# Performance work log

Measured on AMD Instinct MI355X. Metric: run time of the kernel, lower is better.

The kernel has to match this reference:

```python
import jax, jax.numpy as jnp
import numpy as np

N, K, H, HEADS, DE, MULT = 8000, 32, 256, 8, 128, 2
DH = H // HEADS
BIG_NEG = -1e9


def _ln(x, g, b):
    mu = x.mean(-1, keepdims=True)
    var = ((x - mu) ** 2).mean(-1, keepdims=True)
    return (x - mu) * jax.lax.rsqrt(var + 1e-5) * g + b


def setup_inputs() -> dict:
    key = jax.random.key(0)
    ks = iter(jax.random.split(key, 64))
    def w(shape, s=0.05):
        return (jax.random.normal(next(ks), shape, jnp.float32) * s)
    stdv = float(np.sqrt(6.0 / (HEADS + DH)))
    inp = {
        'node_features': jax.random.normal(next(ks), (N, H), jnp.float32),
        'edge_features': jax.random.normal(next(ks), (N, K, H), jnp.float32),
        'edge_attr_raw': jax.random.normal(next(ks), (N, K, DE), jnp.float32),
        'angle_embedding': jax.random.normal(next(ks), (N, HEADS, K, K), jnp.float32) * 0.1,
        'ln1n_g': jnp.ones((H,)), 'ln1n_b': jnp.zeros((H,)),
        'ln1e_g': jnp.ones((H,)), 'ln1e_b': jnp.zeros((H,)),
        'W_ea': w((DE, H)), 'b_ea': jnp.zeros((H,)),
        'W_nh': w((H, H)), 'b_nh': jnp.zeros((H,)),
        'W_eh': w((H, H)), 'b_eh': jnp.zeros((H,)),
        'W_gate': w((2 * H, H)), 'b_gate': jnp.zeros((H,)),
        'W_cand': w((2 * H, H)), 'b_cand': jnp.zeros((H,)),
        'attn_scalar': jnp.ones((HEADS,)),
        'W_in': w((H, 3 * H)), 'b_in': jnp.zeros((3 * H,)),
        'W_out': w((H, H)), 'b_out': jnp.zeros((H,)),
        'attn_weight': jax.random.uniform(next(ks), (HEADS, DH), jnp.float32, -stdv, stdv),
        'ln2n_g': jnp.ones((H,)), 'ln2n_b': jnp.zeros((H,)),
        'ln2e_g': jnp.ones((H,)), 'ln2e_b': jnp.zeros((H,)),
        'Wn1': w((H, MULT * H)), 'bn1': jnp.zeros((MULT * H,)),
        'Wn2': w((MULT * H, H)), 'bn2': jnp.zeros((H,)),
        'We1': w((H, MULT * H)), 'be1': jnp.zeros((MULT * H,)),
        'We2': w((MULT * H, H)), 'be2': jnp.zeros((H,)),
        'neighbor_list': jax.random.randint(next(ks), (N, K), 0, N),
        'neighbor_counts': jax.random.randint(next(ks), (N,), 1, K + 1),
    }
    return inp


def _forward(node_features, edge_features, edge_attr_raw, angle_embedding,
             ln1n_g, ln1n_b, ln1e_g, ln1e_b,
             W_ea, b_ea, W_nh, b_nh, W_eh, b_eh,
             W_gate, b_gate, W_cand, b_cand,
             attn_scalar, W_in, b_in, W_out, b_out, attn_weight,
             ln2n_g, ln2n_b, ln2e_g, ln2e_b,
             Wn1, bn1, Wn2, bn2, We1, be1, We2, be2,
             neighbor_list, neighbor_counts):
    mask = jnp.arange(K)[None, :] < neighbor_counts[:, None]  # [N,K] valid neighbors
    # norm_attn
    nh = _ln(node_features, ln1n_g, ln1n_b)
    eh = _ln(edge_features, ln1e_g, ln1e_b)
    # message construction
    edge_attr = jax.nn.gelu(edge_attr_raw @ W_ea + b_ea)            # [N,K,H]
    nbr = nh[neighbor_list]                                          # gather [N,K,H]
    node_hidden = jax.nn.gelu(nbr @ W_nh + b_nh)
    edge_hidden = jax.nn.gelu(eh @ W_eh + b_eh)
    m = jnp.concatenate([edge_attr, node_hidden], axis=-1)          # [N,K,2H]
    gate = jax.nn.sigmoid(m @ W_gate + b_gate)
    cand = jnp.tanh(m @ W_cand + b_cand)
    message = gate * cand + (1.0 - gate) * edge_hidden              # [N,K,H]
    # additive mask: key padding + per-head scaled angle embedding
    attn_mask = jnp.where(mask[:, None, None, :], 0.0, BIG_NEG) \
        + angle_embedding * attn_scalar[None, :, None, None]        # [N,heads,K,K]
    # multi-head self attention over the neighbor dimension
    qkv = message @ W_in + b_in                                     # [N,K,3H]
    q, k, v = jnp.split(qkv, 3, axis=-1)
    q = q.reshape(N, K, HEADS, DH)
    k = k.reshape(N, K, HEADS, DH)
    v = v.reshape(N, K, HEADS, DH)
    scores = jnp.einsum('nqhd,nkhd->nhqk', q, k) / np.float32(np.sqrt(DH)) + attn_mask
    probs = jax.nn.softmax(scores, axis=-1)
    ctx = jnp.einsum('nhqk,nkhd->nqhd', probs, v).reshape(N, K, H)
    edge_output = ctx @ W_out + b_out                               # [N,K,H]
    # graph-attention aggregation to nodes
    eo = edge_output.reshape(N, K, HEADS, DH)
    alpha = (eo * attn_weight[None, None]).sum(-1)                  # [N,K,heads]
    alpha = jax.nn.leaky_relu(alpha, 0.2)
    alpha = jnp.where(mask[:, :, None], alpha, BIG_NEG)
    alpha = jax.nn.softmax(alpha, axis=1)
    node_output = (alpha[..., None] * eo).sum(1).reshape(N, H)
    # residual + FFN
    node_f = node_output + node_features
    edge_f = edge_output + edge_features
    nh2 = _ln(node_f, ln2n_g, ln2n_b)
    eh2 = _ln(edge_f, ln2e_g, ln2e_b)
    node_f = node_f + (jax.nn.gelu(nh2 @ Wn1 + bn1) @ Wn2 + bn2)
    edge_f = edge_f + (jax.nn.gelu(eh2 @ We1 + be1) @ We2 + be2)
    return node_f, edge_f


def reference(node_features, edge_features, edge_attr_raw, angle_embedding,
              ln1n_g, ln1n_b, ln1e_g, ln1e_b,
              W_ea, b_ea, W_nh, b_nh, W_eh, b_eh,
              W_gate, b_gate, W_cand, b_cand,
              attn_scalar, W_in, b_in, W_out, b_out, attn_weight,
              ln2n_g, ln2n_b, ln2e_g, ln2e_b,
              Wn1, bn1, Wn2, bn2, We1, be1, We2, be2,
              neighbor_list, neighbor_counts):
    return _forward(node_features, edge_features, edge_attr_raw, angle_embedding,
                    ln1n_g, ln1n_b, ln1e_g, ln1e_b,
                    W_ea, b_ea, W_nh, b_nh, W_eh, b_eh,
                    W_gate, b_gate, W_cand, b_cand,
                    attn_scalar, W_in, b_in, W_out, b_out, attn_weight,
                    ln2n_g, ln2n_b, ln2e_g, ln2e_b,
                    Wn1, bn1, Wn2, bn2, We1, be1, We2, be2,
                    neighbor_list, neighbor_counts)
```

## Files before the change

### kernel.cpp

```cpp
#include <hip/hip_runtime.h>
#include <math.h>

#define NN 8000
#define KK 32
#define HH 256
#define DE 128
#define NODES 4
#define THREADS 512
#define BIGLD 536
#define LDS_BYTES (128 * BIGLD * 2)

typedef __attribute__((ext_vector_type(8))) short bs8;
typedef __attribute__((ext_vector_type(4))) short bs4;
typedef __attribute__((ext_vector_type(4))) float f4;

#define LGK_FENCE() do { asm volatile("s_waitcnt lgkmcnt(0)" ::: "memory"); __builtin_amdgcn_sched_barrier(0); } while (0)

struct P {
  const float *nf, *ef, *ear, *ang;
  const float *ln1e_g, *ln1e_b;
  const float *b_ea, *b_nh, *b_eh, *b_gate, *b_cand;
  const float *ascal, *b_in, *b_out, *aw;
  const float *ln2n_g, *ln2n_b, *ln2e_g, *ln2e_b;
  const float *bn1, *bn2, *be1, *be2;
  const int *nbrl, *nbrc;
  const unsigned short *nhb;
  const unsigned short *wtEA, *wtNH, *wtEH, *wtG, *wtC, *wtIN, *wtOUT, *wtN1, *wtN2, *wtE1, *wtE2;
  float *on, *oe;
};

__device__ __forceinline__ unsigned short f2b(float f) {
  unsigned int u = __float_as_uint(f);
  unsigned int r = (u + 0x7fffu + ((u >> 16) & 1u)) >> 16;
  return (unsigned short)r;
}
__device__ __forceinline__ float b2f(unsigned short u) {
  return __uint_as_float(((unsigned int)u) << 16);
}
__device__ __forceinline__ unsigned int cvt_pk_bf16(float lo, float hi) {
  unsigned int r;
  asm("v_cvt_pk_bf16_f32 %0, %1, %2" : "=v"(r) : "v"(lo), "v"(hi));
  return r;
}
__device__ __forceinline__ bs4 pack4(float a, float b, float c, float d) {
  union { unsigned int u[2]; bs4 v; } x;
  x.u[0] = cvt_pk_bf16(a, b);
  x.u[1] = cvt_pk_bf16(c, d);
  return x.v;
}
__device__ __forceinline__ float fast_tanh(float x) {
  x = fminf(fmaxf(x, -12.f), 12.f);
  float e = __expf(2.f * x);
  return (e - 1.f) / (e + 1.f);
}
__device__ __forceinline__ float gelu_f(float x) {
  return 0.5f * x * (1.f + fast_tanh(0.7978845608f * (x + 0.044715f * x * x * x)));
}
__device__ __forceinline__ float sigmoid_f(float x) {
  return 1.f / (1.f + __expf(-x));
}

template<int RT, int NCT, int KB, int KW>
__device__ __forceinline__ void gemmB(f4 acc[RT][NCT],
    const unsigned short* __restrict__ wt,
    const unsigned short* __restrict__ A, int cs, int l)
{
  const int lm = l & 15;
  const int lg = (l >> 4) << 3;
  #pragma unroll
  for (int kb = 0; kb < KB; ++kb) {
    bs8 wfr[NCT];
    #pragma unroll
    for (int ct = 0; ct < NCT; ++ct)
      wfr[ct] = *(const bs8*)(wt + (size_t)(cs + ct * 16 + lm) * KW + kb * 32 + lg);
    bs8 afr[RT];
    #pragma unroll
    for (int rt = 0; rt < RT; ++rt)
      afr[rt] = *(const bs8*)(A + (rt * 16 + lm) * BIGLD + kb * 32 + lg);
    #pragma unroll
    for (int rt = 0; rt < RT; ++rt)
      #pragma unroll
      for (int ct = 0; ct < NCT; ++ct)
        acc[rt][ct] = __builtin_amdgcn_mfma_f32_16x16x32_bf16(wfr[ct], afr[rt], acc[rt][ct], 0, 0, 0);
  }
}

template<int RT, int NCT>
__device__ __forceinline__ void zero_acc(f4 acc[RT][NCT]) {
  #pragma unroll
  for (int rt = 0; rt < RT; ++rt)
    #pragma unroll
    for (int ct = 0; ct < NCT; ++ct) {
      acc[rt][ct][0] = 0.f; acc[rt][ct][1] = 0.f; acc[rt][ct][2] = 0.f; acc[rt][ct][3] = 0.f;
    }
}

template<int RT, int NCT, int ACTF>
__device__ __forceinline__ void storeB(unsigned short* dst,
    f4 acc[RT][NCT], const float* __restrict__ bias, int cs, int l)
{
  const int lm = l & 15;
  const int lr = (l >> 4) << 2;
  #pragma unroll
  for (int ct = 0; ct < NCT; ++ct) {
    f4 bv = *(const f4*)(bias + cs + ct * 16 + lr);
    #pragma unroll
    for (int rt = 0; rt < RT; ++rt) {
      float v[4];
      #pragma unroll
      for (int r = 0; r < 4; ++r) {
        v[r] = acc[rt][ct][r] + bv[r];
        if (ACTF == 1) v[r] = gelu_f(v[r]);
      }
      *(bs4*)(dst + (rt * 16 + lm) * BIGLD + cs + ct * 16 + lr) = pack4(v[0], v[1], v[2], v[3]);
    }
  }
}

__global__ void node_ln_bf16(const float* __restrict__ x, const float* __restrict__ g,
                             const float* __restrict__ b, unsigned short* __restrict__ y)
{
  int row = blockIdx.x * 4 + (threadIdx.x >> 6);
  int lane = threadIdx.x & 63;
  float4 v = ((const float4*)(x + (size_t)row * HH))[lane];
  float s = v.x + v.y + v.z + v.w;
  float ss = v.x * v.x + v.y * v.y + v.z * v.z + v.w * v.w;
  #pragma unroll
  for (int m = 1; m < 64; m <<= 1) { s += __shfl_xor(s, m); ss += __shfl_xor(ss, m); }
  float mean = s * (1.f / HH);
  float var = ss * (1.f / HH) - mean * mean;
  float rstd = rsqrtf(var + 1e-5f);
  float4 gg = ((const float4*)g)[lane];
  float4 bb = ((const float4*)b)[lane];
  *(bs4*)(y + (size_t)row * HH + lane * 4) =
      pack4((v.x - mean) * rstd * gg.x + bb.x, (v.y - mean) * rstd * gg.y + bb.y,
            (v.z - mean) * rstd * gg.z + bb.z, (v.w - mean) * rstd * gg.w + bb.w);
}

__global__ void wt_transpose(const float* __restrict__ src, unsigned short* __restrict__ dst,
                             int K, int C)
{
  __shared__ float tile[32][33];
  int tx = threadIdx.x & 31, ty = threadIdx.x >> 5;
  int bk = blockIdx.x, bc = blockIdx.y;
  #pragma unroll
  for (int i = 0; i < 4; ++i)
    tile[ty + i * 8][tx] = src[(size_t)(bk * 32 + ty + i * 8) * C + bc * 32 + tx];
  __syncthreads();
  #pragma unroll
  for (int i = 0; i < 4; ++i)
    dst[(size_t)(bc * 32 + ty + i * 8) * K + bk * 32 + tx] = f2b(tile[tx][ty + i * 8]);
}

__launch_bounds__(THREADS, 2)
__global__ void mega_kernel(P p)
{
  extern __shared__ unsigned short smem[];

  const int tid = threadIdx.x;
  const int l = tid & 63;
  const int w = tid >> 6;
  const int lm = l & 15;
  const int lg = (l >> 4) << 3;
  const int lr = (l >> 4) << 2;
  const int n0 = blockIdx.x * NODES;
  const size_t ebase = (size_t)blockIdx.x * 128;
  const int4 cnt4 = *(const int4*)(p.nbrc + n0);
  const int cnts[4] = { cnt4.x, cnt4.y, cnt4.z, cnt4.w };

  #define FSA(i)  (*(float*)(smem + ((i) >> 7) * BIGLD + 256 + (((i) & 127) << 1)))
  #define FSNF(i) (*(float*)(smem + (8 + ((i) >> 7)) * BIGLD + 256 + (((i) & 127) << 1)))
  #define FLNP(j) (*(float*)(smem + 16 * BIGLD + 256 + ((j) << 1)))

  {
    int row = tid >> 2, q = tid & 3;
    const float* src = p.ear + (ebase + row) * DE + q * 32;
    unsigned short* d = smem + row * BIGLD + q * 32;
    #pragma unroll
    for (int j = 0; j < 8; ++j) {
      float4 v = ((const float4*)src)[j];
      *(bs4*)(d + j * 4) = pack4(v.x, v.y, v.z, v.w);
    }
  }
  __syncthreads();
  {
    f4 acc[8][2]; zero_acc<8,2>(acc);
    gemmB<8,2,4,128>(acc, p.wtEA, smem, w * 32, l);
    __syncthreads();
    storeB<8,2,1>(smem, acc, p.b_ea, w * 32, l);
  }
  __syncthreads();
  {
    int row = tid >> 2, q = tid & 3;
    int idx = p.nbrl[(n0 + (row >> 5)) * KK + (row & 31)];
    const unsigned short* src = p.nhb + (size_t)idx * HH + q * 64;
    unsigned short* d = smem + row * BIGLD + 264 + q * 64;
    #pragma unroll
    for (int j = 0; j < 8; ++j) *(bs8*)(d + j * 8) = *(const bs8*)(src + j * 8);
  }
  __syncthreads();
  {
    f4 acc[8][2]; zero_acc<8,2>(acc);
    gemmB<8,2,8,256>(acc, p.wtNH, smem + 264, w * 32, l);
    __syncthreads();
    storeB<8,2,1>(smem + 256, acc, p.b_nh, w * 32, l);
  }
  __syncthreads();
  bs4 gp[8][2], cp[8][2];
  {
    f4 ga[8][2]; zero_acc<8,2>(ga);
    f4 ca[8][2]; zero_acc<8,2>(ca);
    gemmB<8,2,16,512>(ga, p.wtG, smem, w * 32, l);
    gemmB<8,2,16,512>(ca, p.wtC, smem, w * 32, l);
    #pragma unroll
    for (int ct = 0; ct < 2; ++ct) {
      f4 bg = *(const f4*)(p.b_gate + w * 32 + ct * 16 + lr);
      f4 bc = *(const f4*)(p.b_cand + w * 32 + ct * 16 + lr);
      #pragma unroll
      for (int rt = 0; rt < 8; ++rt) {
        gp[rt][ct] = pack4(sigmoid_f(ga[rt][ct][0] + bg[0]), sigmoid_f(ga[rt][ct][1] + bg[1]),
                           sigmoid_f(ga[rt][ct][2] + bg[2]), sigmoid_f(ga[rt][ct][3] + bg[3]));
        cp[rt][ct] = pack4(fast_tanh(ca[rt][ct][0] + bc[0]), fast_tanh(ca[rt][ct][1] + bc[1]),
                           fast_tanh(ca[rt][ct][2] + bc[2]), fast_tanh(ca[rt][ct][3] + bc[3]));
      }
    }
  }
  __syncthreads();
  {
    int row = tid >> 2, q = tid & 3;
    const float* src = p.ef + (ebase + row) * HH + q * 64;
    float s = 0.f, ss = 0.f;
    #pragma unroll
    for (int j = 0; j < 16; ++j) {
      float4 v = ((const float4*)src)[j];
      s += v.x + v.y + v.z + v.w;
      ss += v.x * v.x + v.y * v.y + v.z * v.z + v.w * v.w;
    }
    s += __shfl_xor(s, 1); ss += __shfl_xor(ss, 1);
    s += __shfl_xor(s, 2); ss += __shfl_xor(ss, 2);
    float mean = s * (1.f / HH);
    float var = ss * (1.f / HH) - mean * mean;
    float rstd = rsqrtf(var + 1e-5f);
    unsigned short* d = smem + row * BIGLD + q * 64;
    #pragma unroll
    for (int j = 0; j < 16; ++j) {
      float4 v = ((const float4*)src)[j];
      int c = q * 64 + j * 4;
      float4 g = *(const float4*)(p.ln1e_g + c);
      float4 b = *(const float4*)(p.ln1e_b + c);
      *(bs4*)(d + j * 4) = pack4((v.x - mean) * rstd * g.x + b.x,
                                 (v.y - mean) * rstd * g.y + b.y,
                                 (v.z - mean) * rstd * g.z + b.z,
                                 (v.w - mean) * rstd * g.w + b.w);
    }
  }
  __syncthreads();
  {
    f4 ea[8][2]; zero_acc<8,2>(ea);
    gemmB<8,2,8,256>(ea, p.wtEH, smem, w * 32, l);
    __syncthreads();
    #pragma unroll
    for (int ct = 0; ct < 2; ++ct) {
      f4 be = *(const f4*)(p.b_eh + w * 32 + ct * 16 + lr);
      #pragma unroll
      for (int rt = 0; rt < 8; ++rt) {
        float o[4];
        #pragma unroll
        for (int r = 0; r < 4; ++r) {
          float g = b2f((unsigned short)gp[rt][ct][r]);
          float c = b2f((unsigned short)cp[rt][ct][r]);
          float eh = gelu_f(ea[rt][ct][r] + be[r]);
          o[r] = g * c + (1.f - g) * eh;
        }
        *(bs4*)(smem + (rt * 16 + lm) * BIGLD + w * 32 + ct * 16 + lr) = pack4(o[0], o[1], o[2], o[3]);
      }
    }
  }
  __syncthreads();
  bs4 qp[8][2], kp[8][2], vp[8][2];
  {
    f4 acc[8][2];
    zero_acc<8,2>(acc);
    gemmB<8,2,8,256>(acc, p.wtIN, smem, w * 32, l);
    #pragma unroll
    for (int ct = 0; ct < 2; ++ct) {
      f4 bv = *(const f4*)(p.b_in + w * 32 + ct * 16 + lr);
      #pragma unroll
      for (int rt = 0; rt < 8; ++rt)
        qp[rt][ct] = pack4(acc[rt][ct][0] + bv[0], acc[rt][ct][1] + bv[1],
                           acc[rt][ct][2] + bv[2], acc[rt][ct][3] + bv[3]);
    }
    zero_acc<8,2>(acc);
    gemmB<8,2,8,256>(acc, p.wtIN + 256 * 256, smem, w * 32, l);
    #pragma unroll
    for (int ct = 0; ct < 2; ++ct) {
      f4 bv = *(const f4*)(p.b_in + 256 + w * 32 + ct * 16 + lr);
      #pragma unroll
      for (int rt = 0; rt < 8; ++rt)
        kp[rt][ct] = pack4(acc[rt][ct][0] + bv[0], acc[rt][ct][1] + bv[1],
                           acc[rt][ct][2] + bv[2], acc[rt][ct][3] + bv[3]);
    }
    zero_acc<8,2>(acc);
    gemmB<8,2,8,256>(acc, p.wtIN + 512 * 256, smem, w * 32, l);
    #pragma unroll
    for (int ct = 0; ct < 2; ++ct) {
      f4 bv = *(const f4*)(p.b_in + 512 + w * 32 + ct * 16 + lr);
      #pragma unroll
      for (int rt = 0; rt < 8; ++rt)
        vp[rt][ct] = pack4(acc[rt][ct][0] + bv[0], acc[rt][ct][1] + bv[1],
                           acc[rt][ct][2] + bv[2], acc[rt][ct][3] + bv[3]);
    }
  }
  __syncthreads();
  bs4 cxp[NODES][2][2];
  {
    const float asc = p.ascal[w];
    f4 z; z[0] = 0.f; z[1] = 0.f; z[2] = 0.f; z[3] = 0.f;
    #define WSADDR(a, r, c) ((w * 8 + (a) * 4 + ((r) >> 3)) * BIGLD + 256 + (((r) & 7) << 5) + (c))
    #pragma unroll
    for (int ni = 0; ni < NODES; ++ni) {
      #pragma unroll
      for (int j = 0; j < 2; ++j)
        #pragma unroll
        for (int ct = 0; ct < 2; ++ct) {
          *(bs4*)(smem + WSADDR(0, j * 16 + lm, ct * 16 + lr)) = qp[2 * ni + j][ct];
          *(bs4*)(smem + WSADDR(1, j * 16 + lm, ct * 16 + lr)) = kp[2 * ni + j][ct];
        }
      LGK_FENCE();
      bs8 qf[2], kf[2];
      #pragma unroll
      for (int t = 0; t < 2; ++t) {
        qf[t] = *(const bs8*)(smem + WSADDR(0, t * 16 + lm, lg));
        kf[t] = *(const bs8*)(smem + WSADDR(1, t * 16 + lm, lg));
      }
      f4 sc[2][2];
      #pragma unroll
      for (int kt = 0; kt < 2; ++kt)
        #pragma unroll
        for (int qt = 0; qt < 2; ++qt)
          sc[kt][qt] = __builtin_amdgcn_mfma_f32_16x16x32_bf16(kf[kt], qf[qt], z, 0, 0, 0);
      float inv[2];
      #pragma unroll
      for (int qt = 0; qt < 2; ++qt) {
        const int q = qt * 16 + lm;
        float sv[2][4];
        #pragma unroll
        for (int kt = 0; kt < 2; ++kt) {
          f4 av = *(const f4*)(p.ang + ((((size_t)(n0 + ni)) * 8 + w) * 32 + q) * 32 + kt * 16 + lr);
          #pragma unroll
          for (int r = 0; r < 4; ++r) {
            int kidx = kt * 16 + lr + r;
            sv[kt][r] = sc[kt][qt][r] * 0.17677669529663687f + av[r] * asc
                      + (kidx < cnts[ni] ? 0.f : -1e9f);
          }
        }
        float m = sv[0][0];
        #pragma unroll
        for (int r = 1; r < 4; ++r) m = fmaxf(m, sv[0][r]);
        #pragma unroll
        for (int r = 0; r < 4; ++r) m = fmaxf(m, sv[1][r]);
        m = fmaxf(m, __shfl_xor(m, 16));
        m = fmaxf(m, __shfl_xor(m, 32));
        float e[2][4], sum = 0.f;
        #pragma unroll
        for (int kt = 0; kt < 2; ++kt)
          #pragma unroll
          for (int r = 0; r < 4; ++r) { e[kt][r] = __expf(sv[kt][r] - m); sum += e[kt][r]; }
        sum += __shfl_xor(sum, 16);
        sum += __shfl_xor(sum, 32);
        inv[qt] = 1.f / sum;
        *(bs4*)(smem + WSADDR(0, q, lr))      = pack4(e[0][0], e[0][1], e[0][2], e[0][3]);
        *(bs4*)(smem + WSADDR(0, q, 16 + lr)) = pack4(e[1][0], e[1][1], e[1][2], e[1][3]);
      }
      #pragma unroll
      for (int j = 0; j < 2; ++j)
        #pragma unroll
        for (int ct = 0; ct < 2; ++ct)
          #pragma unroll
          for (int r = 0; r < 4; ++r)
            smem[WSADDR(1, ct * 16 + lr + r, j * 16 + lm)] = (unsigned short)vp[2 * ni + j][ct][r];
      LGK_FENCE();
      bs8 pf[2], vf[2];
      #pragma unroll
      for (int t = 0; t < 2; ++t) {
        pf[t] = *(const bs8*)(smem + WSADDR(0, t * 16 + lm, lg));
        vf[t] = *(const bs8*)(smem + WSADDR(1, t * 16 + lm, lg));
      }
      #pragma unroll
      for (int qt = 0; qt < 2; ++qt)
        #pragma unroll
        for (int dt = 0; dt < 2; ++dt) {
          f4 cx = __builtin_amdgcn_mfma_f32_16x16x32_bf16(vf[dt], pf[qt], z, 0, 0, 0);
          cxp[ni][qt][dt] = pack4(cx[0] * inv[qt], cx[1] * inv[qt], cx[2] * inv[qt], cx[3] * inv[qt]);
        }
    }
    #undef WSADDR
  }
  __syncthreads();
  {
    #pragma unroll
    for (int ni = 0; ni < NODES; ++ni)
      #pragma unroll
      for (int qt = 0; qt < 2; ++qt)
        #pragma unroll
        for (int dt = 0; dt < 2; ++dt)
          *(bs4*)(smem + (ni * 32 + qt * 16 + lm) * BIGLD + 256 + w * 32 + dt * 16 + lr) = cxp[ni][qt][dt];
  }
  __syncthreads();
  {
    f4 acc[8][2]; zero_acc<8,2>(acc);
    gemmB<8,2,8,256>(acc, p.wtOUT, smem + 256, w * 32, l);
    __syncthreads();
    storeB<8,2,0>(smem, acc, p.b_out, w * 32, l);
  }
  __syncthreads();
  {
    #pragma unroll
    for (int it = 0; it < 2; ++it) {
      int idx = tid + it * 512;
      int ni = idx >> 8, rem = idx & 255;
      int k = rem >> 3, h = rem & 7;
      float aa = 0.f;
      #pragma unroll
      for (int j = 0; j < 8; ++j) {
        bs4 ev = *(const bs4*)(smem + (ni * 32 + k) * BIGLD + h * 32 + j * 4);
        float4 av = *(const float4*)(p.aw + h * 32 + j * 4);
        aa += b2f((unsigned short)ev[0]) * av.x + b2f((unsigned short)ev[1]) * av.y
            + b2f((unsigned short)ev[2]) * av.z + b2f((unsigned short)ev[3]) * av.w;
      }
      aa = aa > 0.f ? aa : 0.2f * aa;
      if (k >= cnts[ni]) aa = -1e9f;
      FSA(idx) = aa;
    }
  }
  __syncthreads();
  {
    int ni = tid >> 7, h = (tid >> 4) & 7, l16 = tid & 15;
    float v0 = FSA(ni * 256 + l16 * 8 + h);
    float v1 = FSA(ni * 256 + (l16 + 16) * 8 + h);
    float m = fmaxf(v0, v1);
    m = fmaxf(m, __shfl_xor(m, 1));
    m = fmaxf(m, __shfl_xor(m, 2));
    m = fmaxf(m, __shfl_xor(m, 4));
    m = fmaxf(m, __shfl_xor(m, 8));
    float e0 = __expf(v0 - m), e1 = __expf(v1 - m);
    float s = e0 + e1;
    s += __shfl_xor(s, 1);
    s += __shfl_xor(s, 2);
    s += __shfl_xor(s, 4);
    s += __shfl_xor(s, 8);
    float inv = 1.f / s;
    FSA(ni * 256 + l16 * 8 + h) = e0 * inv;
    FSA(ni * 256 + (l16 + 16) * 8 + h) = e1 * inv;
  }
  __syncthreads();
  float ndf[2];
  {
    #pragma unroll
    for (int it = 0; it < 2; ++it) {
      int idx = it * 512 + tid;
      int ni = idx >> 8, c = idx & 255, h = c >> 5;
      float no = 0.f;
      #pragma unroll
      for (int k = 0; k < 32; ++k)
        no = fmaf(FSA(ni * 256 + k * 8 + h), b2f(smem[(ni * 32 + k) * BIGLD + c]), no);
      float nodef = no + p.nf[(size_t)(n0 + ni) * HH + c];
      ndf[it] = nodef;
      FSNF(idx) = nodef;
      float s = nodef, ss = nodef * nodef;
      #pragma unroll
      for (int m = 1; m < 64; m <<= 1) { s += __shfl_xor(s, m); ss += __shfl_xor(ss, m); }
      if (l == 0) { FLNP(it * 8 + w) = s; FLNP(16 + it * 8 + w) = ss; }
    }
  }
  __syncthreads();
  {
    #pragma unroll
    for (int it = 0; it < 2; ++it) {
      int idx = it * 512 + tid;
      int ni = idx >> 8, c = idx & 255;
      int base = it * 8 + (ni & 1) * 4;
      float S  = FLNP(base) + FLNP(base + 1) + FLNP(base + 2) + FLNP(base + 3);
      float SS = FLNP(16 + base) + FLNP(16 + base + 1) + FLNP(16 + base + 2) + FLNP(16 + base + 3);
      float mean = S * (1.f / HH), var = SS * (1.f / HH) - mean * mean;
      float rstd = rsqrtf(var + 1e-5f);
      smem[(17 + ni) * BIGLD + 256 + c] = f2b((ndf[it] - mean) * rstd * p.ln2n_g[c] + p.ln2n_b[c]);
    }
    #pragma unroll
    for (int z = 0; z < 3; ++z) {
      int zi = z * 512 + tid;
      int zr = 21 + (zi >> 7), zc = (zi & 127) << 1;
      *(unsigned int*)(smem + zr * BIGLD + 256 + zc) = 0u;
    }
  }
  __syncthreads();
  {
    f4 acc[4];
    #pragma unroll
    for (int ct = 0; ct < 4; ++ct) { acc[ct][0]=0.f; acc[ct][1]=0.f; acc[ct][2]=0.f; acc[ct][3]=0.f; }
    #pragma unroll
    for (int kb = 0; kb < 8; ++kb) {
      bs8 afr = *(const bs8*)(smem + (17 + lm) * BIGLD + 256 + kb * 32 + lg);
      #pragma unroll
      for (int ct = 0; ct < 4; ++ct) {
        bs8 wfr = *(const bs8*)(p.wtN1 + (size_t)(w * 64 + ct * 16 + lm) * 256 + kb * 32 + lg);
        acc[ct] = __builtin_amdgcn_mfma_f32_16x16x32_bf16(wfr, afr, acc[ct], 0, 0, 0);
      }
    }
    __syncthreads();
    #pragma unroll
    for (int ct = 0; ct < 4; ++ct) {
      int col = w * 64 + ct * 16 + lr;
      f4 bv = *(const f4*)(p.bn1 + col);
      *(bs4*)(smem + (33 + 2 * lm + (col >= 256 ? 1 : 0)) * BIGLD + 256 + (col & 255)) =
          pack4(gelu_f(acc[ct][0] + bv[0]), gelu_f(acc[ct][1] + bv[1]),
                gelu_f(acc[ct][2] + bv[2]), gelu_f(acc[ct][3] + bv[3]));
    }
  }
  __syncthreads();
  bs4 efp[8][2];
  {
    f4 acc[2];
    #pragma unroll
    for (int ct = 0; ct < 2; ++ct) { acc[ct][0]=0.f; acc[ct][1]=0.f; acc[ct][2]=0.f; acc[ct][3]=0.f; }
    #pragma unroll
    for (int kb = 0; kb < 16; ++kb) {
      bs8 afr = *(const bs8*)(smem + (33 + 2 * lm + (kb >> 3)) * BIGLD + 256 + (kb & 7) * 32 + lg);
      #pragma unroll
      for (int ct = 0; ct < 2; ++ct) {
        bs8 wfr = *(const bs8*)(p.wtN2 + (size_t)(w * 32 + ct * 16 + lm) * 512 + kb * 32 + lg);
        acc[ct] = __builtin_amdgcn_mfma_f32_16x16x32_bf16(wfr, afr, acc[ct], 0, 0, 0);
      }
    }
    if (lm < 4) {
      #pragma unroll
      for (int ct = 0; ct < 2; ++ct) {
        int col = w * 32 + ct * 16 + lr;
        f4 bv = *(const f4*)(p.bn2 + col);
        float4 o;
        o.x = acc[ct][0] + bv[0] + FSNF(lm * 256 + col);
        o.y = acc[ct][1] + bv[1] + FSNF(lm * 256 + col + 1);
        o.z = acc[ct][2] + bv[2] + FSNF(lm * 256 + col + 2);
        o.w = acc[ct][3] + bv[3] + FSNF(lm * 256 + col + 3);
        *(float4*)(p.on + (size_t)(n0 + lm) * HH + col) = o;
      }
    }
    #pragma unroll
    for (int rt = 0; rt < 8; ++rt)
      #pragma unroll
      for (int ct = 0; ct < 2; ++ct) {
        int row = rt * 16 + lm, col = w * 32 + ct * 16 + lr;
        bs4 ov = *(const bs4*)(smem + row * BIGLD + col);
        float4 e = *(const float4*)(p.ef + (ebase + row) * HH + col);
        efp[rt][ct] = pack4(e.x + b2f((unsigned short)ov[0]), e.y + b2f((unsigned short)ov[1]),
                            e.z + b2f((unsigned short)ov[2]), e.w + b2f((unsigned short)ov[3]));
      }
  }
  __syncthreads();
  {
    int row = tid >> 2, q = tid & 3;
    const float* efs = p.ef + (ebase + row) * HH + q * 64;
    const unsigned short* eor = smem + row * BIGLD + q * 64;
    float xv[64];
    float s = 0.f, ss = 0.f;
    #pragma unroll
    for (int j = 0; j < 16; ++j) {
      float4 e = ((const float4*)efs)[j];
      bs4 ov = *(const bs4*)(eor + j * 4);
      float x0 = e.x + b2f((unsigned short)ov[0]);
      float x1 = e.y + b2f((unsigned short)ov[1]);
      float x2 = e.z + b2f((unsigned short)ov[2]);
      float x3 = e.w + b2f((unsigned short)ov[3]);
      xv[j * 4] = x0; xv[j * 4 + 1] = x1; xv[j * 4 + 2] = x2; xv[j * 4 + 3] = x3;
      s += x0 + x1 + x2 + x3;
      ss += x0 * x0 + x1 * x1 + x2 * x2 + x3 * x3;
    }
    s += __shfl_xor(s, 1); ss += __shfl_xor(ss, 1);
    s += __shfl_xor(s, 2); ss += __shfl_xor(ss, 2);
    float mean = s * (1.f / HH);
    float var = ss * (1.f / HH) - mean * mean;
    float rstd = rsqrtf(var + 1e-5f);
    unsigned short* d = smem + row * BIGLD + q * 64;
    #pragma unroll
    for (int j = 0; j < 16; ++j) {
      int c = q * 64 + j * 4;
      float4 g = *(const float4*)(p.ln2e_g + c);
      float4 b = *(const float4*)(p.ln2e_b + c);
      *(bs4*)(d + j * 4) = pack4((xv[j * 4] - mean) * rstd * g.x + b.x,
                                 (xv[j * 4 + 1] - mean) * rstd * g.y + b.y,
                                 (xv[j * 4 + 2] - mean) * rstd * g.z + b.z,
                                 (xv[j * 4 + 3] - mean) * rstd * g.w + b.w);
    }
  }
  __syncthreads();
  f4 oacc[8][2]; zero_acc<8,2>(oacc);
  {
    f4 h[8][2]; zero_acc<8,2>(h);
    gemmB<8,2,8,256>(h, p.wtE1, smem, w * 32, l);
    __syncthreads();
    storeB<8,2,1>(smem + 256, h, p.be1, w * 32, l);
  }
  __syncthreads();
  {
    gemmB<8,2,8,512>(oacc, p.wtE2, smem + 256, w * 32, l);
    f4 h[8][2]; zero_acc<8,2>(h);
    gemmB<8,2,8,256>(h, p.wtE1 + (size_t)256 * 256, smem, w * 32, l);
    __syncthreads();
    storeB<8,2,1>(smem + 256, h, p.be1 + 256, w * 32, l);
  }
  __syncthreads();
  {
    gemmB<8,2,8,512>(oacc, p.wtE2 + 256, smem + 256, w * 32, l);
    #pragma unroll
    for (int ct = 0; ct < 2; ++ct) {
      f4 bv = *(const f4*)(p.be2 + w * 32 + ct * 16 + lr);
      #pragma unroll
      for (int rt = 0; rt < 8; ++rt) {
        int row = rt * 16 + lm;
        float4 o;
        o.x = oacc[rt][ct][0] + bv[0] + b2f((unsigned short)efp[rt][ct][0]);
        o.y = oacc[rt][ct][1] + bv[1] + b2f((unsigned short)efp[rt][ct][1]);
        o.z = oacc[rt][ct][2] + bv[2] + b2f((unsigned short)efp[rt][ct][2]);
        o.w = oacc[rt][ct][3] + bv[3] + b2f((unsigned short)efp[rt][ct][3]);
        *(float4*)(p.oe + (ebase + row) * HH + w * 32 + ct * 16 + lr) = o;
      }
    }
  }
  #undef FSA
  #undef FSNF
  #undef FLNP
}

extern "C" void kernel_launch(void* const* d_in, const int* in_sizes, int n_in,
                              void* d_out, int out_size, void* d_ws, size_t ws_size,
                              hipStream_t stream)
{
  P p;
  p.nf     = (const float*)d_in[0];
  p.ef     = (const float*)d_in[1];
  p.ear    = (const float*)d_in[2];
  p.ang    = (const float*)d_in[3];
  const float* ln1n_g = (const float*)d_in[4];
  const float* ln1n_b = (const float*)d_in[5];
  p.ln1e_g = (const float*)d_in[6];  p.ln1e_b = (const float*)d_in[7];
  const float* W_ea   = (const float*)d_in[8];  p.b_ea   = (const float*)d_in[9];
  const float* W_nh   = (const float*)d_in[10]; p.b_nh   = (const float*)d_in[11];
  const float* W_eh   = (const float*)d_in[12]; p.b_eh   = (const float*)d_in[13];
  const float* W_gate = (const float*)d_in[14]; p.b_gate = (const float*)d_in[15];
  const float* W_cand = (const float*)d_in[16]; p.b_cand = (const float*)d_in[17];
  p.ascal  = (const float*)d_in[18];
  const float* W_in   = (const float*)d_in[19]; p.b_in   = (const float*)d_in[20];
  const float* W_out  = (const float*)d_in[21]; p.b_out  = (const float*)d_in[22];
  p.aw     = (const float*)d_in[23];
  p.ln2n_g = (const float*)d_in[24]; p.ln2n_b = (const float*)d_in[25];
  p.ln2e_g = (const float*)d_in[26]; p.ln2e_b = (const float*)d_in[27];
  const float* Wn1 = (const float*)d_in[28]; p.bn1 = (const float*)d_in[29];
  const float* Wn2 = (const float*)d_in[30]; p.bn2 = (const float*)d_in[31];
  const float* We1 = (const float*)d_in[32]; p.be1 = (const float*)d_in[33];
  const float* We2 = (const float*)d_in[34]; p.be2 = (const float*)d_in[35];
  p.nbrl   = (const int*)d_in[36];
  p.nbrc   = (const int*)d_in[37];
  p.on     = (float*)d_out;
  p.oe     = (float*)d_out + (size_t)NN * HH;

  size_t off = 0;
  auto alloc = [&](size_t elems) {
    unsigned short* q = (unsigned short*)((char*)d_ws + off);
    off += elems * 2;
    return q;
  };
  unsigned short* nhb = alloc((size_t)NN * HH);
  unsigned short* wtEA  = alloc(256 * 128);
  unsigned short* wtNH  = alloc(256 * 256);
  unsigned short* wtEH  = alloc(256 * 256);
  unsigned short* wtG   = alloc(256 * 512);
  unsigned short* wtC   = alloc(256 * 512);
  unsigned short* wtIN  = alloc(768 * 256);
  unsigned short* wtOUT = alloc(256 * 256);
  unsigned short* wtN1  = alloc(512 * 256);
  unsigned short* wtN2  = alloc(256 * 512);
  unsigned short* wtE1  = alloc(512 * 256);
  unsigned short* wtE2  = alloc(256 * 512);
  p.nhb = nhb;
  p.wtEA = wtEA; p.wtNH = wtNH; p.wtEH = wtEH; p.wtG = wtG; p.wtC = wtC;
  p.wtIN = wtIN; p.wtOUT = wtOUT; p.wtN1 = wtN1; p.wtN2 = wtN2; p.wtE1 = wtE1; p.wtE2 = wtE2;

  node_ln_bf16<<<NN / 4, 256, 0, stream>>>((const float*)d_in[0], ln1n_g, ln1n_b, nhb);

  auto tr = [&](const float* src, unsigned short* dst, int K, int C) {
    wt_transpose<<<dim3(K / 32, C / 32), 256, 0, stream>>>(src, dst, K, C);
  };
  tr(W_ea, wtEA, 128, 256);
  tr(W_nh, wtNH, 256, 256);
  tr(W_eh, wtEH, 256, 256);
  tr(W_gate, wtG, 512, 256);
  tr(W_cand, wtC, 512, 256);
  tr(W_in, wtIN, 256, 768);
  tr(W_out, wtOUT, 256, 256);
  tr(Wn1, wtN1, 256, 512);
  tr(Wn2, wtN2, 512, 256);
  tr(We1, wtE1, 256, 512);
  tr(We2, wtE2, 512, 256);

  (void)hipFuncSetAttribute((const void*)mega_kernel,
                            hipFuncAttributeMaxDynamicSharedMemorySize, LDS_BYTES);
  mega_kernel<<<NN / NODES, THREADS, LDS_BYTES, stream>>>(p);
}
```

Measured before the change: 1.618 ms.

## Halve nodes per block to shrink LDS and raise occupancy

Processes 2 nodes (64 edge rows) per block instead of 4, halving LDS and register tile sizes and raising launch bounds to 4 blocks per CU. Also fuses the edge-attr and neighbor-gather loads into one phase and runs the EA and NH GEMMs back to back, removing two barriers. The trade is that each weight fragment loaded from global/L2 is reused across half as many rows, so weight traffic per edge doubles, and the small-node MLP now uses only 2 of 16 MFMA rows.

```diff
diff --git a/kernel.cpp b/kernel.cpp
--- a/kernel.cpp
+++ b/kernel.cpp
@@ -5,10 +5,11 @@
 #define KK 32
 #define HH 256
 #define DE 128
-#define NODES 4
+#define NODES 2
 #define THREADS 512
 #define BIGLD 536
-#define LDS_BYTES (128 * BIGLD * 2)
+#define ROWS 64
+#define LDS_BYTES (ROWS * BIGLD * 2)
 
 typedef __attribute__((ext_vector_type(8))) short bs8;
 typedef __attribute__((ext_vector_type(4))) short bs4;
@@ -152,7 +153,7 @@
     dst[(size_t)(bc * 32 + ty + i * 8) * K + bk * 32 + tx] = f2b(tile[tx][ty + i * 8]);
 }
 
-__launch_bounds__(THREADS, 2)
+__launch_bounds__(THREADS, 4)
 __global__ void mega_kernel(P p)
 {
   extern __shared__ unsigned short smem[];
@@ -164,60 +165,52 @@
   const int lg = (l >> 4) << 3;
   const int lr = (l >> 4) << 2;
   const int n0 = blockIdx.x * NODES;
-  const size_t ebase = (size_t)blockIdx.x * 128;
-  const int4 cnt4 = *(const int4*)(p.nbrc + n0);
-  const int cnts[4] = { cnt4.x, cnt4.y, cnt4.z, cnt4.w };
+  const size_t ebase = (size_t)blockIdx.x * ROWS;
+  const int2 cnt2 = *(const int2*)(p.nbrc + n0);
+  const int cnts[2] = { cnt2.x, cnt2.y };
 
   #define FSA(i)  (*(float*)(smem + ((i) >> 7) * BIGLD + 256 + (((i) & 127) << 1)))
-  #define FSNF(i) (*(float*)(smem + (8 + ((i) >> 7)) * BIGLD + 256 + (((i) & 127) << 1)))
-  #define FLNP(j) (*(float*)(smem + 16 * BIGLD + 256 + ((j) << 1)))
-
-  {
-    int row = tid >> 2, q = tid & 3;
-    const float* src = p.ear + (ebase + row) * DE + q * 32;
-    unsigned short* d = smem + row * BIGLD + q * 32;
-    #pragma unroll
-    for (int j = 0; j < 8; ++j) {
+  #define FSNF(i) (*(float*)(smem + (4 + ((i) >> 7)) * BIGLD + 256 + (((i) & 127) << 1)))
+  #define FLNP(j) (*(float*)(smem + 8 * BIGLD + 256 + ((j) << 1)))
+
+  {
+    int row = tid >> 3, q = tid & 7;
+    const float* src = p.ear + (ebase + row) * DE + q * 16;
+    unsigned short* d = smem + row * BIGLD + q * 16;
+    #pragma unroll
+    for (int j = 0; j < 4; ++j) {
       float4 v = ((const float4*)src)[j];
       *(bs4*)(d + j * 4) = pack4(v.x, v.y, v.z, v.w);
     }
-  }
-  __syncthreads();
-  {
-    f4 acc[8][2]; zero_acc<8,2>(acc);
-    gemmB<8,2,4,128>(acc, p.wtEA, smem, w * 32, l);
+    int idx = p.nbrl[(n0 + (row >> 5)) * KK + (row & 31)];
+    const unsigned short* gsrc = p.nhb + (size_t)idx * HH + q * 32;
+    unsigned short* gd = smem + row * BIGLD + 264 + q * 32;
+    #pragma unroll
+    for (int j = 0; j < 4; ++j) *(bs8*)(gd + j * 8) = *(const bs8*)(gsrc + j * 8);
+  }
+  __syncthreads();
+  {
+    f4 accA[4][2]; zero_acc<4,2>(accA);
+    gemmB<4,2,4,128>(accA, p.wtEA, smem, w * 32, l);
+    f4 accN[4][2]; zero_acc<4,2>(accN);
+    gemmB<4,2,8,256>(accN, p.wtNH, smem + 264, w * 32, l);
     __syncthreads();
-    storeB<8,2,1>(smem, acc, p.b_ea, w * 32, l);
-  }
-  __syncthreads();
-  {
-    int row = tid >> 2, q = tid & 3;
-    int idx = p.nbrl[(n0 + (row >> 5)) * KK + (row & 31)];
-    const unsigned short* src = p.nhb + (size_t)idx * HH + q * 64;
-    unsigned short* d = smem + row * BIGLD + 264 + q * 64;
-    #pragma unroll
-    for (int j = 0; j < 8; ++j) *(bs8*)(d + j * 8) = *(const bs8*)(src + j * 8);
-  }
-  __syncthreads();
-  {
-    f4 acc[8][2]; zero_acc<8,2>(acc);
-    gemmB<8,2,8,256>(acc, p.wtNH, smem + 264, w * 32, l);
-    __syncthreads();
-    storeB<8,2,1>(smem + 256, acc, p.b_nh, w * 32, l);
-  }
-  __syncthreads();
-  bs4 gp[8][2], cp[8][2];
-  {
-    f4 ga[8][2]; zero_acc<8,2>(ga);
-    f4 ca[8][2]; zero_acc<8,2>(ca);
-    gemmB<8,2,16,512>(ga, p.wtG, smem, w * 32, l);
-    gemmB<8,2,16,512>(ca, p.wtC, smem, w * 32, l);
+    storeB<4,2,1>(smem, accA, p.b_ea, w * 32, l);
+    storeB<4,2,1>(smem + 256, accN, p.b_nh, w * 32, l);
+  }
+  __syncthreads();
+  bs4 gp[4][2], cp[4][2];
+  {
+    f4 ga[4][2]; zero_acc<4,2>(ga);
+    f4 ca[4][2]; zero_acc<4,2>(ca);
+    gemmB<4,2,16,512>(ga, p.wtG, smem, w * 32, l);
+    gemmB<4,2,16,512>(ca, p.wtC, smem, w * 32, l);
     #pragma unroll
     for (int ct = 0; ct < 2; ++ct) {
       f4 bg = *(const f4*)(p.b_gate + w * 32 + ct * 16 + lr);
       f4 bc = *(const f4*)(p.b_cand + w * 32 + ct * 16 + lr);
       #pragma unroll
-      for (int rt = 0; rt < 8; ++rt) {
+      for (int rt = 0; rt < 4; ++rt) {
         gp[rt][ct] = pack4(sigmoid_f(ga[rt][ct][0] + bg[0]), sigmoid_f(ga[rt][ct][1] + bg[1]),
                            sigmoid_f(ga[rt][ct][2] + bg[2]), sigmoid_f(ga[rt][ct][3] + bg[3]));
         cp[rt][ct] = pack4(fast_tanh(ca[rt][ct][0] + bc[0]), fast_tanh(ca[rt][ct][1] + bc[1]),
@@ -227,25 +220,26 @@
   }
   __syncthreads();
   {
-    int row = tid >> 2, q = tid & 3;
-    const float* src = p.ef + (ebase + row) * HH + q * 64;
+    int row = tid >> 3, q = tid & 7;
+    const float* src = p.ef + (ebase + row) * HH + q * 32;
     float s = 0.f, ss = 0.f;
     #pragma unroll
-    for (int j = 0; j < 16; ++j) {
+    for (int j = 0; j < 8; ++j) {
       float4 v = ((const float4*)src)[j];
       s += v.x + v.y + v.z + v.w;
       ss += v.x * v.x + v.y * v.y + v.z * v.z + v.w * v.w;
     }
     s += __shfl_xor(s, 1); ss += __shfl_xor(ss, 1);
     s += __shfl_xor(s, 2); ss += __shfl_xor(ss, 2);
+    s += __shfl_xor(s, 4); ss += __shfl_xor(ss, 4);
     float mean = s * (1.f / HH);
     float var = ss * (1.f / HH) - mean * mean;
     float rstd = rsqrtf(var + 1e-5f);
-    unsigned short* d = smem + row * BIGLD + q * 64;
-    #pragma unroll
-    for (int j = 0; j < 16; ++j) {
+    unsigned short* d = smem + row * BIGLD + q * 32;
+    #pragma unroll
+    for (int j = 0; j < 8; ++j) {
       float4 v = ((const float4*)src)[j];
-      int c = q * 64 + j * 4;
+      int c = q * 32 + j * 4;
       float4 g = *(const float4*)(p.ln1e_g + c);
       float4 b = *(const float4*)(p.ln1e_b + c);
       *(bs4*)(d + j * 4) = pack4((v.x - mean) * rstd * g.x + b.x,
@@ -256,14 +250,14 @@
   }
   __syncthreads();
   {
-    f4 ea[8][2]; zero_acc<8,2>(ea);
-    gemmB<8,2,8,256>(ea, p.wtEH, smem, w * 32, l);
+    f4 ea[4][2]; zero_acc<4,2>(ea);
+    gemmB<4,2,8,256>(ea, p.wtEH, smem, w * 32, l);
     __syncthreads();
     #pragma unroll
     for (int ct = 0; ct < 2; ++ct) {
       f4 be = *(const f4*)(p.b_eh + w * 32 + ct * 16 + lr);
       #pragma unroll
-      for (int rt = 0; rt < 8; ++rt) {
+      for (int rt = 0; rt < 4; ++rt) {
         float o[4];
         #pragma unroll
         for (int r = 0; r < 4; ++r) {
@@ -277,36 +271,36 @@
     }
   }
   __syncthreads();
-  bs4 qp[8][2], kp[8][2], vp[8][2];
-  {
-    f4 acc[8][2];
-    zero_acc<8,2>(acc);
-    gemmB<8,2,8,256>(acc, p.wtIN, smem, w * 32, l);
+  bs4 qp[4][2], kp[4][2], vp[4][2];
+  {
+    f4 acc[4][2];
+    zero_acc<4,2>(acc);
+    gemmB<4,2,8,256>(acc, p.wtIN, smem, w * 32, l);
     #pragma unroll
     for (int ct = 0; ct < 2; ++ct) {
       f4 bv = *(const f4*)(p.b_in + w * 32 + ct * 16 + lr);
       #pragma unroll
-      for (int rt = 0; rt < 8; ++rt)
+      for (int rt = 0; rt < 4; ++rt)
         qp[rt][ct] = pack4(acc[rt][ct][0] + bv[0], acc[rt][ct][1] + bv[1],
                            acc[rt][ct][2] + bv[2], acc[rt][ct][3] + bv[3]);
     }
-    zero_acc<8,2>(acc);
-    gemmB<8,2,8,256>(acc, p.wtIN + 256 * 256, smem, w * 32, l);
+    zero_acc<4,2>(acc);
+    gemmB<4,2,8,256>(acc, p.wtIN + 256 * 256, smem, w * 32, l);
     #pragma unroll
     for (int ct = 0; ct < 2; ++ct) {
       f4 bv = *(const f4*)(p.b_in + 256 + w * 32 + ct * 16 + lr);
       #pragma unroll
-      for (int rt = 0; rt < 8; ++rt)
+      for (int rt = 0; rt < 4; ++rt)
         kp[rt][ct] = pack4(acc[rt][ct][0] + bv[0], acc[rt][ct][1] + bv[1],
                            acc[rt][ct][2] + bv[2], acc[rt][ct][3] + bv[3]);
     }
-    zero_acc<8,2>(acc);
-    gemmB<8,2,8,256>(acc, p.wtIN + 512 * 256, smem, w * 32, l);
+    zero_acc<4,2>(acc);
+    gemmB<4,2,8,256>(acc, p.wtIN + 512 * 256, smem, w * 32, l);
     #pragma unroll
     for (int ct = 0; ct < 2; ++ct) {
       f4 bv = *(const f4*)(p.b_in + 512 + w * 32 + ct * 16 + lr);
       #pragma unroll
-      for (int rt = 0; rt < 8; ++rt)
+      for (int rt = 0; rt < 4; ++rt)
         vp[rt][ct] = pack4(acc[rt][ct][0] + bv[0], acc[rt][ct][1] + bv[1],
                            acc[rt][ct][2] + bv[2], acc[rt][ct][3] + bv[3]);
     }
@@ -408,33 +402,29 @@
   }
   __syncthreads();
   {
-    f4 acc[8][2]; zero_acc<8,2>(acc);
-    gemmB<8,2,8,256>(acc, p.wtOUT, smem + 256, w * 32, l);
+    f4 acc[4][2]; zero_acc<4,2>(acc);
+    gemmB<4,2,8,256>(acc, p.wtOUT, smem + 256, w * 32, l);
     __syncthreads();
-    storeB<8,2,0>(smem, acc, p.b_out, w * 32, l);
-  }
-  __syncthreads();
-  {
-    #pragma unroll
-    for (int it = 0; it < 2; ++it) {
-      int idx = tid + it * 512;
-      int ni = idx >> 8, rem = idx & 255;
-      int k = rem >> 3, h = rem & 7;
-      float aa = 0.f;
-      #pragma unroll
-      for (int j = 0; j < 8; ++j) {
-        bs4 ev = *(const bs4*)(smem + (ni * 32 + k) * BIGLD + h * 32 + j * 4);
-        float4 av = *(const float4*)(p.aw + h * 32 + j * 4);
-        aa += b2f((unsigned short)ev[0]) * av.x + b2f((unsigned short)ev[1]) * av.y
-            + b2f((unsigned short)ev[2]) * av.z + b2f((unsigned short)ev[3]) * av.w;
-      }
-      aa = aa > 0.f ? aa : 0.2f * aa;
-      if (k >= cnts[ni]) aa = -1e9f;
-      FSA(idx) = aa;
-    }
-  }
-  __syncthreads();
-  {
+    storeB<4,2,0>(smem, acc, p.b_out, w * 32, l);
+  }
+  __syncthreads();
+  {
+    int ni = tid >> 8, rem = tid & 255;
+    int k = rem >> 3, h = rem & 7;
+    float aa = 0.f;
+    #pragma unroll
+    for (int j = 0; j < 8; ++j) {
+      bs4 ev = *(const bs4*)(smem + (ni * 32 + k) * BIGLD + h * 32 + j * 4);
+      float4 av = *(const float4*)(p.aw + h * 32 + j * 4);
+      aa += b2f((unsigned short)ev[0]) * av.x + b2f((unsigned short)ev[1]) * av.y
+          + b2f((unsigned short)ev[2]) * av.z + b2f((unsigned short)ev[3]) * av.w;
+    }
+    aa = aa > 0.f ? aa : 0.2f * aa;
+    if (k >= cnts[ni]) aa = -1e9f;
+    FSA(tid) = aa;
+  }
+  __syncthreads();
+  if (tid < 256) {
     int ni = tid >> 7, h = (tid >> 4) & 7, l16 = tid & 15;
     float v0 = FSA(ni * 256 + l16 * 8 + h);
     float v1 = FSA(ni * 256 + (l16 + 16) * 8 + h);
@@ -454,43 +444,35 @@
     FSA(ni * 256 + (l16 + 16) * 8 + h) = e1 * inv;
   }
   __syncthreads();
-  float ndf[2];
-  {
-    #pragma unroll
-    for (int it = 0; it < 2; ++it) {
-      int idx = it * 512 + tid;
-      int ni = idx >> 8, c = idx & 255, h = c >> 5;
-      float no = 0.f;
-      #pragma unroll
-      for (int k = 0; k < 32; ++k)
-        no = fmaf(FSA(ni * 256 + k * 8 + h), b2f(smem[(ni * 32 + k) * BIGLD + c]), no);
-      float nodef = no + p.nf[(size_t)(n0 + ni) * HH + c];
-      ndf[it] = nodef;
-      FSNF(idx) = nodef;
-      float s = nodef, ss = nodef * nodef;
-      #pragma unroll
-      for (int m = 1; m < 64; m <<= 1) { s += __shfl_xor(s, m); ss += __shfl_xor(ss, m); }
-      if (l == 0) { FLNP(it * 8 + w) = s; FLNP(16 + it * 8 + w) = ss; }
-    }
-  }
-  __syncthreads();
-  {
-    #pragma unroll
-    for (int it = 0; it < 2; ++it) {
-      int idx = it * 512 + tid;
-      int ni = idx >> 8, c = idx & 255;
-      int base = it * 8 + (ni & 1) * 4;
-      float S  = FLNP(base) + FLNP(base + 1) + FLNP(base + 2) + FLNP(base + 3);
-      float SS = FLNP(16 + base) + FLNP(16 + base + 1) + FLNP(16 + base + 2) + FLNP(16 + base + 3);
-      float mean = S * (1.f / HH), var = SS * (1.f / HH) - mean * mean;
-      float rstd = rsqrtf(var + 1e-5f);
-      smem[(17 + ni) * BIGLD + 256 + c] = f2b((ndf[it] - mean) * rstd * p.ln2n_g[c] + p.ln2n_b[c]);
-    }
-    #pragma unroll
-    for (int z = 0; z < 3; ++z) {
+  float ndf;
+  {
+    int ni = tid >> 8, c = tid & 255, h = c >> 5;
+    float no = 0.f;
+    #pragma unroll
+    for (int k = 0; k < 32; ++k)
+      no = fmaf(FSA(ni * 256 + k * 8 + h), b2f(smem[(ni * 32 + k) * BIGLD + c]), no);
+    ndf = no + p.nf[(size_t)(n0 + ni) * HH + c];
+    FSNF(tid) = ndf;
+    float s = ndf, ss = ndf * ndf;
+    #pragma unroll
+    for (int m = 1; m < 64; m <<= 1) { s += __shfl_xor(s, m); ss += __shfl_xor(ss, m); }
+    if (l == 0) { FLNP(w) = s; FLNP(8 + w) = ss; }
+  }
+  __syncthreads();
+  {
+    int ni = tid >> 8, c = tid & 255;
+    float S  = FLNP(ni * 4) + FLNP(ni * 4 + 1) + FLNP(ni * 4 + 2) + FLNP(ni * 4 + 3);
+    float SS = FLNP(8 + ni * 4) + FLNP(8 + ni * 4 + 1) + FLNP(8 + ni * 4 + 2) + FLNP(8 + ni * 4 + 3);
+    float mean = S * (1.f / HH), var = SS * (1.f / HH) - mean * mean;
+    float rstd = rsqrtf(var + 1e-5f);
+    smem[(16 + ni) * BIGLD + 256 + c] = f2b((ndf - mean) * rstd * p.ln2n_g[c] + p.ln2n_b[c]);
+    #pragma unroll
+    for (int z = 0; z < 4; ++z) {
       int zi = z * 512 + tid;
-      int zr = 21 + (zi >> 7), zc = (zi & 127) << 1;
-      *(unsigned int*)(smem + zr * BIGLD + 256 + zc) = 0u;
+      if (zi < 1792) {
+        int zr = 18 + (zi >> 7), zc = (zi & 127) << 1;
+        *(unsigned int*)(smem + zr * BIGLD + 256 + zc) = 0u;
+      }
     }
   }
   __syncthreads();
@@ -500,7 +482,7 @@
     for (int ct = 0; ct < 4; ++ct) { acc[ct][0]=0.f; acc[ct][1]=0.f; acc[ct][2]=0.f; acc[ct][3]=0.f; }
     #pragma unroll
     for (int kb = 0; kb < 8; ++kb) {
-      bs8 afr = *(const bs8*)(smem + (17 + lm) * BIGLD + 256 + kb * 32 + lg);
+      bs8 afr = *(const bs8*)(smem + (16 + lm) * BIGLD + 256 + kb * 32 + lg);
       #pragma unroll
       for (int ct = 0; ct < 4; ++ct) {
         bs8 wfr = *(const bs8*)(p.wtN1 + (size_t)(w * 64 + ct * 16 + lm) * 256 + kb * 32 + lg);
@@ -512,27 +494,27 @@
     for (int ct = 0; ct < 4; ++ct) {
       int col = w * 64 + ct * 16 + lr;
       f4 bv = *(const f4*)(p.bn1 + col);
-      *(bs4*)(smem + (33 + 2 * lm + (col >= 256 ? 1 : 0)) * BIGLD + 256 + (col & 255)) =
+      *(bs4*)(smem + (32 + 2 * lm + (col >= 256 ? 1 : 0)) * BIGLD + 256 + (col & 255)) =
           pack4(gelu_f(acc[ct][0] + bv[0]), gelu_f(acc[ct][1] + bv[1]),
                 gelu_f(acc[ct][2] + bv[2]), gelu_f(acc[ct][3] + bv[3]));
     }
   }
   __syncthreads();
-  bs4 efp[8][2];
+  bs4 efp[4][2];
   {
     f4 acc[2];
     #pragma unroll
     for (int ct = 0; ct < 2; ++ct) { acc[ct][0]=0.f; acc[ct][1]=0.f; acc[ct][2]=0.f; acc[ct][3]=0.f; }
     #pragma unroll
     for (int kb = 0; kb < 16; ++kb) {
-      bs8 afr = *(const bs8*)(smem + (33 + 2 * lm + (kb >> 3)) * BIGLD + 256 + (kb & 7) * 32 + lg);
+      bs8 afr = *(const bs8*)(smem + (32 + 2 * lm + (kb >> 3)) * BIGLD + 256 + (kb & 7) * 32 + lg);
       #pragma unroll
       for (int ct = 0; ct < 2; ++ct) {
         bs8 wfr = *(const bs8*)(p.wtN2 + (size_t)(w * 32 + ct * 16 + lm) * 512 + kb * 32 + lg);
         acc[ct] = __builtin_amdgcn_mfma_f32_16x16x32_bf16(wfr, afr, acc[ct], 0, 0, 0);
       }
     }
-    if (lm < 4) {
+    if (lm < NODES) {
       #pragma unroll
       for (int ct = 0; ct < 2; ++ct) {
         int col = w * 32 + ct * 16 + lr;
@@ -546,7 +528,7 @@
       }
     }
     #pragma unroll
-    for (int rt = 0; rt < 8; ++rt)
+    for (int rt = 0; rt < 4; ++rt)
       #pragma unroll
       for (int ct = 0; ct < 2; ++ct) {
         int row = rt * 16 + lm, col = w * 32 + ct * 16 + lr;
@@ -558,13 +540,13 @@
   }
   __syncthreads();
   {
-    int row = tid >> 2, q = tid & 3;
-    const float* efs = p.ef + (ebase + row) * HH + q * 64;
-    const unsigned short* eor = smem + row * BIGLD + q * 64;
-    float xv[64];
+    int row = tid >> 3, q = tid & 7;
+    const float* efs = p.ef + (ebase + row) * HH + q * 32;
+    const unsigned short* eor = smem + row * BIGLD + q * 32;
+    float xv[32];
     float s = 0.f, ss = 0.f;
     #pragma unroll
-    for (int j = 0; j < 16; ++j) {
+    for (int j = 0; j < 8; ++j) {
       float4 e = ((const float4*)efs)[j];
       bs4 ov = *(const bs4*)(eor + j * 4);
       float x0 = e.x + b2f((unsigned short)ov[0]);
@@ -577,13 +559,14 @@
     }
     s += __shfl_xor(s, 1); ss += __shfl_xor(ss, 1);
     s += __shfl_xor(s, 2); ss += __shfl_xor(ss, 2);
+    s += __shfl_xor(s, 4); ss += __shfl_xor(ss, 4);
     float mean = s * (1.f / HH);
     float var = ss * (1.f / HH) - mean * mean;
     float rstd = rsqrtf(var + 1e-5f);
-    unsigned short* d = smem + row * BIGLD + q * 64;
-    #pragma unroll
-    for (int j = 0; j < 16; ++j) {
-      int c = q * 64 + j * 4;
+    unsigned short* d = smem + row * BIGLD + q * 32;
+    #pragma unroll
+    for (int j = 0; j < 8; ++j) {
+      int c = q * 32 + j * 4;
       float4 g = *(const float4*)(p.ln2e_g + c);
       float4 b = *(const float4*)(p.ln2e_b + c);
       *(bs4*)(d + j * 4) = pack4((xv[j * 4] - mean) * rstd * g.x + b.x,
@@ -593,29 +576,29 @@
     }
   }
   __syncthreads();
-  f4 oacc[8][2]; zero_acc<8,2>(oacc);
-  {
-    f4 h[8][2]; zero_acc<8,2>(h);
-    gemmB<8,2,8,256>(h, p.wtE1, smem, w * 32, l);
+  f4 oacc[4][2]; zero_acc<4,2>(oacc);
+  {
+    f4 h[4][2]; zero_acc<4,2>(h);
+    gemmB<4,2,8,256>(h, p.wtE1, smem, w * 32, l);
     __syncthreads();
-    storeB<8,2,1>(smem + 256, h, p.be1, w * 32, l);
-  }
-  __syncthreads();
-  {
-    gemmB<8,2,8,512>(oacc, p.wtE2, smem + 256, w * 32, l);
-    f4 h[8][2]; zero_acc<8,2>(h);
-    gemmB<8,2,8,256>(h, p.wtE1 + (size_t)256 * 256, smem, w * 32, l);
+    storeB<4,2,1>(smem + 256, h, p.be1, w * 32, l);
+  }
+  __syncthreads();
+  {
+    gemmB<4,2,8,512>(oacc, p.wtE2, smem + 256, w * 32, l);
+    f4 h[4][2]; zero_acc<4,2>(h);
+    gemmB<4,2,8,256>(h, p.wtE1 + (size_t)256 * 256, smem, w * 32, l);
     __syncthreads();
-    storeB<8,2,1>(smem + 256, h, p.be1 + 256, w * 32, l);
-  }
-  __syncthreads();
-  {
-    gemmB<8,2,8,512>(oacc, p.wtE2 + 256, smem + 256, w * 32, l);
+    storeB<4,2,1>(smem + 256, h, p.be1 + 256, w * 32, l);
+  }
+  __syncthreads();
+  {
+    gemmB<4,2,8,512>(oacc, p.wtE2 + 256, smem + 256, w * 32, l);
     #pragma unroll
     for (int ct = 0; ct < 2; ++ct) {
       f4 bv = *(const f4*)(p.be2 + w * 32 + ct * 16 + lr);
       #pragma unroll
-      for (int rt = 0; rt < 8; ++rt) {
+      for (int rt = 0; rt < 4; ++rt) {
         int row = rt * 16 + lm;
         float4 o;
         o.x = oacc[rt][ct][0] + bv[0] + b2f((unsigned short)efp[rt][ct][0]);
```

Measured after the change: 1.995 ms. 1.23x slower.
